# Optimization experiments

Hardware: AMD Instinct MI355X
Metric: run time of the kernel (lower is better)

## Reference

```python
import math
import jax, jax.numpy as jnp
import numpy as np

D = 1024
B, L = 4, 4096


def _linear(x, W, b):
    # torch nn.Linear convention: y = x @ W.T + b, W: (out, in)
    return jnp.einsum('bld,ed->ble', x, W) + b


def _ma_k_activation(x, k=0.02):
    x = x / math.sqrt(x.shape[-1])
    return jax.nn.sigmoid(x * k)


def _ma_q_activation(x):
    x = -x / math.sqrt(x.shape[-1])
    return -jnp.where(x >= 0, x, 0.02 * x)  # -leaky_relu(x, 0.02)


def setup_inputs() -> dict:
    key = jax.random.key(0)
    ks = jax.random.split(key, 9)
    s = 1.0 / math.sqrt(D)
    return {
        'x': jax.random.normal(ks[0], (B, L, D), dtype=jnp.float32),
        'Wq1': jax.random.uniform(ks[1], (D, D), jnp.float32, -s, s),
        'bq1': jax.random.uniform(ks[2], (D,), jnp.float32, -s, s),
        'Wk1': jax.random.uniform(ks[3], (D, D), jnp.float32, -s, s),
        'bk1': jax.random.uniform(ks[4], (D,), jnp.float32, -s, s),
        'Wk2': jax.random.uniform(ks[5], (D, D), jnp.float32, -s, s),
        'bk2': jax.random.uniform(ks[6], (D,), jnp.float32, -s, s),
        'Wproj': jax.random.uniform(ks[7], (D, D), jnp.float32, -s, s),
        'bproj': jax.random.uniform(ks[8], (D,), jnp.float32, -s, s),
    }


def reference(x, Wq1, bq1, Wk1, bk1, Wk2, bk2, Wproj, bproj):
    V = x
    # AR branch: exponential keys, normalized running average, sigmoid query gate
    K = jnp.exp(_linear(x, Wk1, bk1))                      # (B,L,D)
    K_cum = jnp.cumsum(K, axis=1) + 1e-6
    S = jnp.cumsum(K * V, axis=1) / K_cum
    Q = jax.nn.sigmoid(_linear(x, Wq1, bq1))
    O_ar = S * Q
    # MA branch: residual errors gated by shifted (q,k) activations
    zero = jnp.zeros_like(x[:, :1, :])
    E = jnp.concatenate([zero, V[:, 1:, :] - O_ar[:, :-1, :]], axis=1)
    qk2_in = jnp.concatenate([zero, x[:, :-1, :]], axis=1)
    K2 = _ma_k_activation(_linear(qk2_in, Wk2, bk2))
    S2 = jnp.cumsum(K2 * E, axis=1)
    Q2 = _ma_q_activation(Q)
    Q2 = jnp.concatenate([zero, Q2[:, :-1, :]], axis=1)
    O_ma = S2 * Q2
    return _linear(O_ar + O_ma, Wproj, bproj)
```

## Files before the change

kernel.cpp:

```cpp
#include <hip/hip_runtime.h>

#define D_DIM 1024
#define L_DIM 4096
#define B_DIM 4
#define M_DIM (B_DIM * L_DIM)
#define N1    3072
#define CHUNKS 64
#define LC     64
#define KDIM  1024
#define NKT   16

using f32x4  = __attribute__((ext_vector_type(4))) float;
using bf16x8 = __attribute__((ext_vector_type(8))) short;

__device__ __forceinline__ unsigned short f2bf(float f) {
    unsigned u = __float_as_uint(f);
    u += 0x7fffu + ((u >> 16) & 1u);
    return (unsigned short)(u >> 16);
}
__device__ __forceinline__ float bf2f(unsigned short h) {
    return __uint_as_float(((unsigned)h) << 16);
}
__device__ __forceinline__ float sigmoidf_(float x) {
    return 1.0f / (1.0f + __expf(-x));
}

__global__ void cvt_bf16_kernel(const float* __restrict__ in, unsigned short* __restrict__ out, int n) {
    int i = (blockIdx.x * blockDim.x + threadIdx.x) * 4;
    if (i < n) {
        float4 v = *reinterpret_cast<const float4*>(in + i);
        uint2 p;
        p.x = (unsigned)f2bf(v.x) | ((unsigned)f2bf(v.y) << 16);
        p.y = (unsigned)f2bf(v.z) | ((unsigned)f2bf(v.w) << 16);
        *reinterpret_cast<uint2*>(out + i) = p;
    }
}

__device__ __forceinline__ void gld_lds16(const void* g, void* s) {
    __builtin_amdgcn_global_load_lds((const __attribute__((address_space(1))) void*)g,
                                     (__attribute__((address_space(3))) void*)s, 16, 0, 0);
}

#define BAR()  do { asm volatile("" ::: "memory"); __builtin_amdgcn_s_barrier(); asm volatile("" ::: "memory"); } while (0)
#define MFMA16(a_, b_, c_) __builtin_amdgcn_mfma_f32_16x16x32_bf16(a_, b_, c_, 0, 0, 0)

__global__ __launch_bounds__(512, 2) void gemm256(
        const unsigned short* __restrict__ A, const unsigned short* __restrict__ Bm,
        unsigned short* __restrict__ Cb, float* __restrict__ Cf,
        const float* __restrict__ bb0, const float* __restrict__ bb1, const float* __restrict__ bb2,
        int nwgDiv8, int mode) {
    extern __shared__ __align__(16) short lds[];
    const int tid  = threadIdx.x;
    const int wid  = tid >> 6, lane = tid & 63;
    const int wr   = wid >> 2, wc = wid & 3;
    const int lr   = lane & 15, kg = lane >> 4;

    int lin = blockIdx.y * 64 + blockIdx.x;
    int swz = (lin & 7) * nwgDiv8 + (lin >> 3);
    int bm = swz & 63;
    int bn = swz >> 6;
    const size_t rowA0 = (size_t)bm * 256;
    const size_t rowB0 = (size_t)bn * 256;

    const int rh = tid >> 2;
    const int sl = (tid & 3) ^ ((rh >> 1) & 3);
    const int wbase = (tid >> 6) * 512;
    const size_t aoffG = (size_t)rh * KDIM + sl * 8;

#define STAGE(Mp_, row0_, kt_, kh_, c_, mat_, cur_) \
    gld_lds16((Mp_) + ((row0_) + (size_t)(c_) * 128) * KDIM + (size_t)(kt_) * 64 + (kh_) * 32 + aoffG, \
              (void*)(lds + (cur_) * 32768 + (mat_) * 16384 + (kh_) * 8192 + (c_) * 4096 + wbase))

    const int slotR = kg ^ ((lr >> 1) & 3);
    const int aRd = (wr * 128 + lr) * 32 + slotR * 8;
    const int bRd = (wc * 64  + lr) * 32 + slotR * 8;

    f32x4 acc[8][4];
#pragma unroll
    for (int i = 0; i < 8; ++i)
#pragma unroll
        for (int j = 0; j < 4; ++j) acc[i][j] = (f32x4){0.f, 0.f, 0.f, 0.f};

    STAGE(A,  rowA0, 0, 0, 0, 0, 0); STAGE(A,  rowA0, 0, 0, 1, 0, 0);
    STAGE(Bm, rowB0, 0, 0, 0, 1, 0); STAGE(Bm, rowB0, 0, 0, 1, 1, 0);
    STAGE(A,  rowA0, 0, 1, 0, 0, 0); STAGE(A,  rowA0, 0, 1, 1, 0, 0);
    STAGE(Bm, rowB0, 0, 1, 0, 1, 0); STAGE(Bm, rowB0, 0, 1, 1, 1, 0);
    STAGE(A,  rowA0, 1, 0, 0, 0, 1); STAGE(A,  rowA0, 1, 0, 1, 0, 1);
    STAGE(Bm, rowB0, 1, 0, 0, 1, 1); STAGE(Bm, rowB0, 1, 0, 1, 1, 1);
    asm volatile("s_waitcnt vmcnt(4)" ::: "memory");
    BAR();

    for (int kt = 0; kt < NKT; ++kt) {
        const int cur = kt & 1;
        const short* A0 = lds + cur * 32768;
        const short* A1 = A0 + 8192;
        const short* B0 = A0 + 16384;
        const short* B1 = A0 + 24576;
        bf16x8 a[8], b0, b1, b2, b3;

        #pragma unroll
        for (int fm = 0; fm < 8; ++fm) a[fm] = *reinterpret_cast<const bf16x8*>(A0 + aRd + fm * 512);
        b0 = *reinterpret_cast<const bf16x8*>(B0 + bRd);
        b1 = *reinterpret_cast<const bf16x8*>(B0 + bRd + 512);
        if (kt + 1 < NKT) {
            const int nc = cur ^ 1;
            STAGE(A,  rowA0, kt + 1, 1, 0, 0, nc); STAGE(A,  rowA0, kt + 1, 1, 1, 0, nc);
            STAGE(Bm, rowB0, kt + 1, 1, 0, 1, nc); STAGE(Bm, rowB0, kt + 1, 1, 1, 1, nc);
        }
        BAR();
        __builtin_amdgcn_s_setprio(1);
        #pragma unroll
        for (int fm = 0; fm < 8; ++fm) {
            acc[fm][0] = MFMA16(a[fm], b0, acc[fm][0]);
            acc[fm][1] = MFMA16(a[fm], b1, acc[fm][1]);
        }
        __builtin_amdgcn_s_setprio(0);
        BAR();

        b2 = *reinterpret_cast<const bf16x8*>(B0 + bRd + 1024);
        b3 = *reinterpret_cast<const bf16x8*>(B0 + bRd + 1536);
        BAR();
        __builtin_amdgcn_s_setprio(1);
        #pragma unroll
        for (int fm = 0; fm < 8; ++fm) {
            acc[fm][2] = MFMA16(a[fm], b2, acc[fm][2]);
            acc[fm][3] = MFMA16(a[fm], b3, acc[fm][3]);
        }
        __builtin_amdgcn_s_setprio(0);
        BAR();

        #pragma unroll
        for (int fm = 0; fm < 8; ++fm) a[fm] = *reinterpret_cast<const bf16x8*>(A1 + aRd + fm * 512);
        b0 = *reinterpret_cast<const bf16x8*>(B1 + bRd);
        b1 = *reinterpret_cast<const bf16x8*>(B1 + bRd + 512);
        if (kt + 2 < NKT) {
            STAGE(A, rowA0, kt + 2, 0, 0, 0, cur); STAGE(A, rowA0, kt + 2, 0, 1, 0, cur);
        }
        BAR();
        __builtin_amdgcn_s_setprio(1);
        #pragma unroll
        for (int fm = 0; fm < 8; ++fm) {
            acc[fm][0] = MFMA16(a[fm], b0, acc[fm][0]);
            acc[fm][1] = MFMA16(a[fm], b1, acc[fm][1]);
        }
        __builtin_amdgcn_s_setprio(0);
        BAR();

        b2 = *reinterpret_cast<const bf16x8*>(B1 + bRd + 1024);
        b3 = *reinterpret_cast<const bf16x8*>(B1 + bRd + 1536);
        if (kt + 2 < NKT) {
            STAGE(Bm, rowB0, kt + 2, 0, 0, 1, cur); STAGE(Bm, rowB0, kt + 2, 0, 1, 1, cur);
        }
        BAR();
        __builtin_amdgcn_s_setprio(1);
        #pragma unroll
        for (int fm = 0; fm < 8; ++fm) {
            acc[fm][2] = MFMA16(a[fm], b2, acc[fm][2]);
            acc[fm][3] = MFMA16(a[fm], b3, acc[fm][3]);
        }
        __builtin_amdgcn_s_setprio(0);
        if (kt < NKT - 2) { asm volatile("s_waitcnt vmcnt(4)" ::: "memory"); }
        else              { asm volatile("s_waitcnt vmcnt(0)" ::: "memory"); }
        BAR();
    }

    const int rowBase = bm * 256 + wr * 128;
    const int colBase = bn * 256 + wc * 64;
    if (mode == 0) {
        const int seg = (colBase >> 10);
        const float* bs = (seg == 0) ? bb0 : ((seg == 1) ? bb1 : bb2);
#pragma unroll
        for (int fn = 0; fn < 4; ++fn) {
            int col = colBase + fn * 16 + lr;
            float bias = bs[col & 1023];
#pragma unroll
            for (int fm = 0; fm < 8; ++fm) {
#pragma unroll
                for (int j = 0; j < 4; ++j) {
                    int row = rowBase + fm * 16 + kg * 4 + j;
                    float v = acc[fm][fn][j] + bias;
                    float rv = (seg == 0) ? __expf(v)
                             : (seg == 1) ? sigmoidf_(v)
                                          : sigmoidf_(v * 6.25e-4f);
                    Cb[(size_t)row * 3072 + col] = f2bf(rv);
                }
            }
        }
    } else {
#pragma unroll
        for (int fn = 0; fn < 4; ++fn) {
            int col = colBase + fn * 16 + lr;
            float bias = bb0[col];
#pragma unroll
            for (int fm = 0; fm < 8; ++fm) {
#pragma unroll
                for (int j = 0; j < 4; ++j) {
                    int row = rowBase + fm * 16 + kg * 4 + j;
                    Cf[(size_t)row * 1024 + col] = acc[fm][fn][j] + bias;
                }
            }
        }
    }
#undef STAGE
}

__global__ void pass1(const unsigned short* __restrict__ KQ, const float* __restrict__ x,
                      float* __restrict__ pK, float* __restrict__ pKV) {
    int tid = blockIdx.x * 256 + threadIdx.x;
    int d  = tid & 1023;
    int bc = tid >> 10;
    size_t row0 = ((size_t)(bc >> 6)) * L_DIM + (size_t)(bc & 63) * LC;
    const unsigned short* kp = KQ + row0 * 3072 + d;
    const float* vp = x + row0 * 1024 + d;
    float sK = 0.f, sKV = 0.f;
#pragma unroll 8
    for (int i = 0; i < LC; ++i) {
        float k = bf2f(kp[(size_t)i * 3072]);
        float v = vp[(size_t)i * 1024];
        sK += k;
        sKV += k * v;
    }
    pK[tid] = sK;
    pKV[tid] = sKV;
}

__global__ void scan_ex2(float* __restrict__ pK, float* __restrict__ pKV) {
    int tid = blockIdx.x * 256 + threadIdx.x;
    int d = tid & 1023, b = tid >> 10;
    float rK = 0.f, rKV = 0.f;
#pragma unroll 8
    for (int c = 0; c < CHUNKS; ++c) {
        size_t i = ((size_t)(b * CHUNKS + c)) * 1024 + d;
        float a = pK[i], q = pKV[i];
        pK[i] = rK; pKV[i] = rKV;
        rK += a; rKV += q;
    }
}

__global__ void scan_ex1(float* __restrict__ p) {
    int tid = blockIdx.x * 256 + threadIdx.x;
    int d = tid & 1023, b = tid >> 10;
    float r = 0.f;
#pragma unroll 8
    for (int c = 0; c < CHUNKS; ++c) {
        size_t i = ((size_t)(b * CHUNKS + c)) * 1024 + d;
        float a = p[i]; p[i] = r; r += a;
    }
}

__global__ void pass3(const unsigned short* __restrict__ KQ, const float* __restrict__ x,
                      const float* __restrict__ oK, const float* __restrict__ oKV,
                      unsigned short* __restrict__ oarB, unsigned short* __restrict__ mB,
                      float* __restrict__ pM) {
    int tid = blockIdx.x * 256 + threadIdx.x;
    int d  = tid & 1023;
    int bc = tid >> 10;
    int c  = bc & 63;
    size_t row0 = ((size_t)(bc >> 6)) * L_DIM + (size_t)c * LC;
    const unsigned short* kqp = KQ + row0 * 3072 + d;
    const float* vp = x + row0 * 1024 + d;
    float cK = oK[tid], cKV = oKV[tid];
    float oar_prev = 0.f;
    if (c != 0) {
        float qm1 = bf2f(kqp[-2048]);
        oar_prev = qm1 * (cKV / (cK + 1e-6f));
    }
    float sM = 0.f;
    {
        float k = bf2f(kqp[0]);
        float q = bf2f(kqp[1024]);
        float v = vp[0];
        cK += k; cKV += k * v;
        float oar = q * (cKV / (cK + 1e-6f));
        float m = 0.f;
        if (c != 0) {
            float k2 = bf2f(kqp[-1024]);
            m = k2 * (v - oar_prev);
        }
        sM += m;
        size_t gi = row0 * 1024 + d;
        oarB[gi] = f2bf(oar);
        mB[gi]   = f2bf(m);
        oar_prev = oar;
    }
#pragma unroll 4
    for (int i = 1; i < LC; ++i) {
        float k = bf2f(kqp[(size_t)i * 3072]);
        float q = bf2f(kqp[(size_t)i * 3072 + 1024]);
        float v = vp[(size_t)i * 1024];
        cK += k; cKV += k * v;
        float oar = q * (cKV / (cK + 1e-6f));
        float k2 = bf2f(kqp[(size_t)(i - 1) * 3072 + 2048]);
        float m = k2 * (v - oar_prev);
        sM += m;
        size_t gi = (row0 + (size_t)i) * 1024 + d;
        oarB[gi] = f2bf(oar);
        mB[gi]   = f2bf(m);
        oar_prev = oar;
    }
    pM[tid] = sM;
}

__global__ void pass5(const unsigned short* __restrict__ KQ,
                      const unsigned short* __restrict__ oarB, const unsigned short* __restrict__ mB,
                      const float* __restrict__ oM, unsigned short* __restrict__ yin) {
    int tid = blockIdx.x * 256 + threadIdx.x;
    int d  = tid & 1023;
    int bc = tid >> 10;
    int c  = bc & 63;
    size_t row0 = ((size_t)(bc >> 6)) * L_DIM + (size_t)c * LC;
    const unsigned short* qp = KQ + row0 * 3072 + 1024 + d;
    float cM = oM[tid];
    {
        size_t gi = row0 * 1024 + d;
        cM += bf2f(mB[gi]);
        float qm1 = (c == 0) ? 0.f : bf2f(qp[-3072]);
        yin[gi] = f2bf(bf2f(oarB[gi]) + cM * 6.25e-4f * qm1);
    }
#pragma unroll 4
    for (int i = 1; i < LC; ++i) {
        size_t gi = (row0 + (size_t)i) * 1024 + d;
        cM += bf2f(mB[gi]);
        float qm1 = bf2f(qp[(size_t)(i - 1) * 3072]);
        yin[gi] = f2bf(bf2f(oarB[gi]) + cM * 6.25e-4f * qm1);
    }
}

extern "C" void kernel_launch(void* const* d_in, const int* in_sizes, int n_in,
                              void* d_out, int out_size, void* d_ws, size_t ws_size,
                              hipStream_t stream) {
    (void)in_sizes; (void)n_in; (void)out_size; (void)ws_size;
    const float* x   = (const float*)d_in[0];
    const float* Wq1 = (const float*)d_in[1];
    const float* bq1 = (const float*)d_in[2];
    const float* Wk1 = (const float*)d_in[3];
    const float* bk1 = (const float*)d_in[4];
    const float* Wk2 = (const float*)d_in[5];
    const float* bk2 = (const float*)d_in[6];
    const float* Wpj = (const float*)d_in[7];
    const float* bpj = (const float*)d_in[8];
    float* out = (float*)d_out;

    char* ws = (char*)d_ws;
    unsigned short* xbf   = (unsigned short*)(ws);
    unsigned short* Wcat  = (unsigned short*)(ws + 33554432);
    unsigned short* Wpjbf = (unsigned short*)(ws + 39845888);
    unsigned short* KQ    = (unsigned short*)(ws + 41943040);
    unsigned short* oarB  = (unsigned short*)(ws + 142606336);
    unsigned short* mB    = (unsigned short*)(ws + 176160768);
    unsigned short* yin   = (unsigned short*)(ws + 209715200);
    float* pK  = (float*)(ws + 243269632);
    float* pKV = (float*)(ws + 244318208);
    float* pM  = (float*)(ws + 245366784);

    (void)hipFuncSetAttribute((const void*)gemm256,
                              hipFuncAttributeMaxDynamicSharedMemorySize, 131072);

    const int nx = M_DIM * D_DIM;
    const int nw = D_DIM * D_DIM;
    cvt_bf16_kernel<<<nx / 4 / 256, 256, 0, stream>>>(x, xbf, nx);
    cvt_bf16_kernel<<<nw / 4 / 256, 256, 0, stream>>>(Wk1, Wcat, nw);
    cvt_bf16_kernel<<<nw / 4 / 256, 256, 0, stream>>>(Wq1, Wcat + nw, nw);
    cvt_bf16_kernel<<<nw / 4 / 256, 256, 0, stream>>>(Wk2, Wcat + 2 * nw, nw);
    cvt_bf16_kernel<<<nw / 4 / 256, 256, 0, stream>>>(Wpj, Wpjbf, nw);

    gemm256<<<dim3(64, 12), 512, 131072, stream>>>(xbf, Wcat, KQ, nullptr,
                                                   bk1, bq1, bk2, 96, 0);

    pass1<<<M_DIM * D_DIM / LC / 256, 256, 0, stream>>>(KQ, x, pK, pKV);
    scan_ex2<<<16, 256, 0, stream>>>(pK, pKV);
    pass3<<<M_DIM * D_DIM / LC / 256, 256, 0, stream>>>(KQ, x, pK, pKV, oarB, mB, pM);
    scan_ex1<<<16, 256, 0, stream>>>(pM);
    pass5<<<M_DIM * D_DIM / LC / 256, 256, 0, stream>>>(KQ, oarB, mB, pM, yin);

    gemm256<<<dim3(64, 4), 512, 131072, stream>>>(yin, Wpjbf, nullptr, out,
                                                  bpj, nullptr, nullptr, 32, 1);
}
```

Before: 328.3 us.

## Swap MFMA operands for row-contiguous output and vectorize GEMM epilogue stores

```diff
diff --git a/kernel.cpp b/kernel.cpp
--- a/kernel.cpp
+++ b/kernel.cpp
@@ -102,6 +102,8 @@
         for (int fm = 0; fm < 8; ++fm) a[fm] = *reinterpret_cast<const bf16x8*>(A0 + aRd + fm * 512);
         b0 = *reinterpret_cast<const bf16x8*>(B0 + bRd);
         b1 = *reinterpret_cast<const bf16x8*>(B0 + bRd + 512);
+        b2 = *reinterpret_cast<const bf16x8*>(B0 + bRd + 1024);
+        b3 = *reinterpret_cast<const bf16x8*>(B0 + bRd + 1536);
         if (kt + 1 < NKT) {
             const int nc = cur ^ 1;
             STAGE(A,  rowA0, kt + 1, 1, 0, 0, nc); STAGE(A,  rowA0, kt + 1, 1, 1, 0, nc);
@@ -111,20 +113,18 @@
         __builtin_amdgcn_s_setprio(1);
         #pragma unroll
         for (int fm = 0; fm < 8; ++fm) {
-            acc[fm][0] = MFMA16(a[fm], b0, acc[fm][0]);
-            acc[fm][1] = MFMA16(a[fm], b1, acc[fm][1]);
+            acc[fm][0] = MFMA16(b0, a[fm], acc[fm][0]);
+            acc[fm][1] = MFMA16(b1, a[fm], acc[fm][1]);
         }
         __builtin_amdgcn_s_setprio(0);
         BAR();
 
-        b2 = *reinterpret_cast<const bf16x8*>(B0 + bRd + 1024);
-        b3 = *reinterpret_cast<const bf16x8*>(B0 + bRd + 1536);
         BAR();
         __builtin_amdgcn_s_setprio(1);
         #pragma unroll
         for (int fm = 0; fm < 8; ++fm) {
-            acc[fm][2] = MFMA16(a[fm], b2, acc[fm][2]);
-            acc[fm][3] = MFMA16(a[fm], b3, acc[fm][3]);
+            acc[fm][2] = MFMA16(b2, a[fm], acc[fm][2]);
+            acc[fm][3] = MFMA16(b3, a[fm], acc[fm][3]);
         }
         __builtin_amdgcn_s_setprio(0);
         BAR();
@@ -133,30 +133,30 @@
         for (int fm = 0; fm < 8; ++fm) a[fm] = *reinterpret_cast<const bf16x8*>(A1 + aRd + fm * 512);
         b0 = *reinterpret_cast<const bf16x8*>(B1 + bRd);
         b1 = *reinterpret_cast<const bf16x8*>(B1 + bRd + 512);
-        if (kt + 2 < NKT) {
-            STAGE(A, rowA0, kt + 2, 0, 0, 0, cur); STAGE(A, rowA0, kt + 2, 0, 1, 0, cur);
-        }
-        BAR();
-        __builtin_amdgcn_s_setprio(1);
-        #pragma unroll
-        for (int fm = 0; fm < 8; ++fm) {
-            acc[fm][0] = MFMA16(a[fm], b0, acc[fm][0]);
-            acc[fm][1] = MFMA16(a[fm], b1, acc[fm][1]);
-        }
-        __builtin_amdgcn_s_setprio(0);
-        BAR();
-
         b2 = *reinterpret_cast<const bf16x8*>(B1 + bRd + 1024);
         b3 = *reinterpret_cast<const bf16x8*>(B1 + bRd + 1536);
         if (kt + 2 < NKT) {
+            STAGE(A, rowA0, kt + 2, 0, 0, 0, cur); STAGE(A, rowA0, kt + 2, 0, 1, 0, cur);
+        }
+        BAR();
+        __builtin_amdgcn_s_setprio(1);
+        #pragma unroll
+        for (int fm = 0; fm < 8; ++fm) {
+            acc[fm][0] = MFMA16(b0, a[fm], acc[fm][0]);
+            acc[fm][1] = MFMA16(b1, a[fm], acc[fm][1]);
+        }
+        __builtin_amdgcn_s_setprio(0);
+        BAR();
+
+        if (kt + 2 < NKT) {
             STAGE(Bm, rowB0, kt + 2, 0, 0, 1, cur); STAGE(Bm, rowB0, kt + 2, 0, 1, 1, cur);
         }
         BAR();
         __builtin_amdgcn_s_setprio(1);
         #pragma unroll
         for (int fm = 0; fm < 8; ++fm) {
-            acc[fm][2] = MFMA16(a[fm], b2, acc[fm][2]);
-            acc[fm][3] = MFMA16(a[fm], b3, acc[fm][3]);
+            acc[fm][2] = MFMA16(b2, a[fm], acc[fm][2]);
+            acc[fm][3] = MFMA16(b3, a[fm], acc[fm][3]);
         }
         __builtin_amdgcn_s_setprio(0);
         if (kt < NKT - 2) { asm volatile("s_waitcnt vmcnt(4)" ::: "memory"); }
@@ -170,34 +170,43 @@
         const int seg = (colBase >> 10);
         const float* bs = (seg == 0) ? bb0 : ((seg == 1) ? bb1 : bb2);
 #pragma unroll
-        for (int fn = 0; fn < 4; ++fn) {
-            int col = colBase + fn * 16 + lr;
-            float bias = bs[col & 1023];
-#pragma unroll
-            for (int fm = 0; fm < 8; ++fm) {
-#pragma unroll
-                for (int j = 0; j < 4; ++j) {
-                    int row = rowBase + fm * 16 + kg * 4 + j;
-                    float v = acc[fm][fn][j] + bias;
-                    float rv = (seg == 0) ? __expf(v)
-                             : (seg == 1) ? sigmoidf_(v)
-                                          : sigmoidf_(v * 6.25e-4f);
-                    Cb[(size_t)row * 3072 + col] = f2bf(rv);
-                }
+        for (int fm = 0; fm < 8; ++fm) {
+            int row = rowBase + fm * 16 + lr;
+            unsigned short* cp = Cb + (size_t)row * 3072;
+#pragma unroll
+            for (int fn = 0; fn < 4; ++fn) {
+                int col0 = colBase + fn * 16 + kg * 4;
+                float4 b4 = *reinterpret_cast<const float4*>(bs + (col0 & 1023));
+                float v0 = acc[fm][fn][0] + b4.x;
+                float v1 = acc[fm][fn][1] + b4.y;
+                float v2 = acc[fm][fn][2] + b4.z;
+                float v3 = acc[fm][fn][3] + b4.w;
+                float r0, r1, r2, r3;
+                if (seg == 0)      { r0 = __expf(v0); r1 = __expf(v1); r2 = __expf(v2); r3 = __expf(v3); }
+                else if (seg == 1) { r0 = sigmoidf_(v0); r1 = sigmoidf_(v1); r2 = sigmoidf_(v2); r3 = sigmoidf_(v3); }
+                else               { r0 = sigmoidf_(v0 * 6.25e-4f); r1 = sigmoidf_(v1 * 6.25e-4f);
+                                     r2 = sigmoidf_(v2 * 6.25e-4f); r3 = sigmoidf_(v3 * 6.25e-4f); }
+                uint2 p;
+                p.x = (unsigned)f2bf(r0) | ((unsigned)f2bf(r1) << 16);
+                p.y = (unsigned)f2bf(r2) | ((unsigned)f2bf(r3) << 16);
+                *reinterpret_cast<uint2*>(cp + col0) = p;
             }
         }
     } else {
 #pragma unroll
-        for (int fn = 0; fn < 4; ++fn) {
-            int col = colBase + fn * 16 + lr;
-            float bias = bb0[col];
-#pragma unroll
-            for (int fm = 0; fm < 8; ++fm) {
-#pragma unroll
-                for (int j = 0; j < 4; ++j) {
-                    int row = rowBase + fm * 16 + kg * 4 + j;
-                    Cf[(size_t)row * 1024 + col] = acc[fm][fn][j] + bias;
-                }
+        for (int fm = 0; fm < 8; ++fm) {
+            int row = rowBase + fm * 16 + lr;
+            float* cp = Cf + (size_t)row * 1024;
+#pragma unroll
+            for (int fn = 0; fn < 4; ++fn) {
+                int col0 = colBase + fn * 16 + kg * 4;
+                float4 b4 = *reinterpret_cast<const float4*>(bb0 + col0);
+                float4 v;
+                v.x = acc[fm][fn][0] + b4.x;
+                v.y = acc[fm][fn][1] + b4.y;
+                v.z = acc[fm][fn][2] + b4.z;
+                v.w = acc[fm][fn][3] + b4.w;
+                *reinterpret_cast<float4*>(cp + col0) = v;
             }
         }
     }
```

Measured after the change: 315.9 us. 3.8% less time.
